# Optimization experiments

Measured on AMD Instinct MI355X. Metric: run time of the kernel, lower is better.

The kernel has to match this reference:

```python
import jax, jax.numpy as jnp
import numpy as np

B, D = 8192, 128
MARGIN = 0.1
N_CLASSES, N_GROUPS = 64, 8


def setup_inputs() -> dict:
    key = jax.random.key(0)
    k1, k2, k3 = jax.random.split(key, 3)
    embeddings = jax.random.normal(k1, (B, D), dtype=jnp.float32)
    labels = jax.random.randint(k2, (B,), 0, N_CLASSES, dtype=jnp.int64)
    groups = jax.random.randint(k3, (B,), 0, N_GROUPS, dtype=jnp.int64)
    return {"embeddings": embeddings, "labels": labels, "groups": groups}


def reference(embeddings, labels, groups):
    # cosine metric: L2-normalize rows (torch F.normalize eps=1e-12)
    norm = jnp.maximum(jnp.linalg.norm(embeddings, axis=1, keepdims=True), 1e-12)
    x = embeddings / norm
    dist = 1.0 - jnp.matmul(x, x.T)                      # [B, B]

    n = embeddings.shape[0]
    eye = jnp.eye(n, dtype=bool)
    same_label = labels[:, None] == labels[None, :]       # [B, B]
    pos_mask = same_label & ~eye
    neg_mask = ~same_label
    neg_sg_mask = neg_mask & (groups[:, None] == groups[None, :])

    BIG = jnp.float32(1e9)
    # hardest positive per row (masked max), hardest negative per row (masked min)
    dist_ap = jnp.max(jnp.where(pos_mask, dist, -BIG), axis=1)
    dist_an_sg = jnp.min(jnp.where(neg_sg_mask, dist, BIG), axis=1)
    dist_an_all = jnp.min(jnp.where(neg_mask, dist, BIG), axis=1)

    has_pos = jnp.any(pos_mask, axis=1)
    has_neg_sg = jnp.any(neg_sg_mask, axis=1)
    has_neg = jnp.any(neg_mask, axis=1)

    # fallback: same-group negatives preferred, else any negative
    dist_an = jnp.where(has_neg_sg, dist_an_sg, dist_an_all)

    loss = jax.nn.relu(dist_ap - dist_an + MARGIN)        # [B]
    # original only averages strictly-positive losses over valid anchors
    include = has_pos & has_neg & (loss > 0)
    cnt = jnp.sum(include.astype(jnp.float32))
    total = jnp.sum(jnp.where(include, loss, 0.0))
    final = jnp.where(cnt > 0, total / jnp.maximum(cnt, 1.0), 0.0)
    final = jnp.where(jnp.isnan(final), 0.0, final)
    return final
```

## Files before the change

### kernel.cpp

```cpp
#include <hip/hip_runtime.h>
#include <math.h>

#define NB 8192
#define DK 128
#define TI 128
#define NTILES (NB / TI)
#define NBLK (NTILES * (NTILES + 1) / 2)
#define JT 64
#define NT (TI / JT)
#define BSTRH 136
#define NCOMB (NB / 256)

typedef __attribute__((ext_vector_type(8))) short short8;
typedef __attribute__((ext_vector_type(16))) float float16;

__device__ inline unsigned short f2bf(float f) {
    unsigned int x = __float_as_uint(f);
    unsigned int r = (x + 0x7fffu + ((x >> 16) & 1u)) >> 16;
    return (unsigned short)r;
}

__global__ void norm_kernel(const float* __restrict__ emb, const int* __restrict__ labels,
                            const int* __restrict__ groups, unsigned short* __restrict__ xnb,
                            int* __restrict__ meta, float* __restrict__ accum,
                            int* __restrict__ ticket) {
    int row  = blockIdx.x * 4 + (threadIdx.x >> 6);
    int lane = threadIdx.x & 63;
    float2 v = ((const float2*)(emb + (size_t)row * DK))[lane];
    float ss = v.x * v.x + v.y * v.y;
#pragma unroll
    for (int off = 32; off; off >>= 1) ss += __shfl_xor(ss, off, 64);
    float inv = 1.0f / fmaxf(sqrtf(ss), 1e-12f);
    ushort2 o;
    o.x = f2bf(v.x * inv);
    o.y = f2bf(v.y * inv);
    ((ushort2*)(xnb + (size_t)row * DK))[lane] = o;
    if (lane == 0) meta[row] = (labels[row] << 8) | groups[row];
    if (blockIdx.x == 0 && threadIdx.x == 0) {
        accum[0] = 0.0f; accum[1] = 0.0f; ticket[0] = 0;
    }
}

__global__ __launch_bounds__(256, 3) void mine_tri(
    const unsigned short* __restrict__ xnb, const int* __restrict__ meta,
    float2* __restrict__ part) {
    __shared__ unsigned short Bs[JT * BSTRH];

    int bid = blockIdx.x;
    int ti = 0;
    while (bid >= NTILES - ti) { bid -= NTILES - ti; ti++; }
    const int tj = ti + bid;

    const int tid  = threadIdx.x;
    const int w    = tid >> 6;
    const int lane = tid & 63;
    const int half = lane >> 5;
    const int l31  = lane & 31;
    const int i0    = ti * TI;
    const int jbase = tj * TI;
    const int irow  = i0 + w * 32;

    short8 afrag[8];
#pragma unroll
    for (int ks = 0; ks < 8; ks++)
        afrag[ks] = *(const short8*)(xnb + (size_t)(irow + l31) * DK + ks * 16 + half * 8);

    int metaI[16];
    float apn[16], anc[16];
#pragma unroll
    for (int reg = 0; reg < 16; reg++) {
        int r = (reg & 3) + 8 * (reg >> 2) + 4 * half;
        metaI[reg] = meta[irow + r];
        apn[reg] = -1e9f; anc[reg] = -1e9f;
    }
    float apnC[4], ancC[4];
#pragma unroll
    for (int q = 0; q < 4; q++) { apnC[q] = -1e9f; ancC[q] = -1e9f; }

#pragma unroll
    for (int jt = 0; jt < NT; jt++) {
        const int j0 = jbase + jt * JT;

        if (jt) __syncthreads();
#pragma unroll
        for (int s = 0; s < 4; s++) {
            int chunk = tid + s * 256;
            int row = chunk >> 4, k4 = chunk & 15;
            *(uint4*)&Bs[row * BSTRH + k4 * 8] =
                *(const uint4*)(xnb + (size_t)(j0 + row) * DK + k4 * 8);
        }
        __syncthreads();

        int mjc[2];
        mjc[0] = meta[j0 + l31];
        mjc[1] = meta[j0 + 32 + l31];

#pragma unroll
        for (int ct = 0; ct < 2; ct++) {
            float16 c;
#pragma unroll
            for (int e = 0; e < 16; e++) c[e] = 0.0f;

            const int bro = ct * 32 + l31;
#pragma unroll
            for (int ks = 0; ks < 8; ks++) {
                short8 b = *(const short8*)&Bs[bro * BSTRH + ks * 16 + half * 8];
                c = __builtin_amdgcn_mfma_f32_32x32x16_bf16(afrag[ks], b, c, 0, 0, 0);
            }

            const int mj = mjc[ct];
            const int q  = jt * 2 + ct;
#pragma unroll
            for (int reg = 0; reg < 16; reg++) {
                float s = c[reg];
                int x = metaI[reg] ^ mj;
                bool sl = (unsigned)x < 0x100u;
                float t8 = s - 8.0f;
                float t  = sl ? t8 : s;
                float negt = -t;
                apn[reg] = fmaxf(apn[reg], negt);
                apnC[q]  = fmaxf(apnC[q],  negt);
                bool sg = (x & 0xFFu) == 0u;
                float t4 = t + 4.0f;
                float v  = sg ? t4 : t;
                anc[reg] = fmaxf(anc[reg], v);
                ancC[q]  = fmaxf(ancC[q],  v);
            }
        }
    }

#pragma unroll
    for (int reg = 0; reg < 16; reg++) {
#pragma unroll
        for (int off = 16; off; off >>= 1) {
            apn[reg] = fmaxf(apn[reg], __shfl_xor(apn[reg], off, 64));
            anc[reg] = fmaxf(anc[reg], __shfl_xor(anc[reg], off, 64));
        }
    }
    if (l31 == 0) {
#pragma unroll
        for (int reg = 0; reg < 16; reg++) {
            int r = (reg & 3) + 8 * (reg >> 2) + 4 * half;
            float2 o; o.x = apn[reg]; o.y = anc[reg];
            part[(size_t)tj * NB + (irow + r)] = o;
        }
    }

    __syncthreads();
    float* colred = (float*)&Bs[0];
#pragma unroll
    for (int q = 0; q < 4; q++) {
        apnC[q] = fmaxf(apnC[q], __shfl_xor(apnC[q], 32, 64));
        ancC[q] = fmaxf(ancC[q], __shfl_xor(ancC[q], 32, 64));
        if (half == 0) {
            colred[0 * 512 + w * 128 + q * 32 + l31] = apnC[q];
            colred[1 * 512 + w * 128 + q * 32 + l31] = ancC[q];
        }
    }
    __syncthreads();
    if (tid < 128 && ti != tj) {
        int e = tid;
        float ma = -1e9f, mn = -1e9f;
#pragma unroll
        for (int wv = 0; wv < 4; wv++) {
            ma = fmaxf(ma, colred[0 * 512 + wv * 128 + e]);
            mn = fmaxf(mn, colred[1 * 512 + wv * 128 + e]);
        }
        float2 o; o.x = ma; o.y = mn;
        part[(size_t)ti * NB + (jbase + e)] = o;
    }
}

__global__ void combine_kernel(const float2* __restrict__ part,
                               float* __restrict__ accum, int* __restrict__ ticket,
                               float* __restrict__ out) {
    int i = blockIdx.x * 256 + threadIdx.x;
    float a0 = -1e9f, a1 = -1e9f, a2 = -1e9f, a3 = -1e9f;
    float n0 = -1e9f, n1 = -1e9f, n2 = -1e9f, n3 = -1e9f;
#pragma unroll
    for (int s = 0; s < NTILES; s += 4) {
        float2 p0 = part[(size_t)(s + 0) * NB + i];
        float2 p1 = part[(size_t)(s + 1) * NB + i];
        float2 p2 = part[(size_t)(s + 2) * NB + i];
        float2 p3 = part[(size_t)(s + 3) * NB + i];
        a0 = fmaxf(a0, p0.x); n0 = fmaxf(n0, p0.y);
        a1 = fmaxf(a1, p1.x); n1 = fmaxf(n1, p1.y);
        a2 = fmaxf(a2, p2.x); n2 = fmaxf(n2, p2.y);
        a3 = fmaxf(a3, p3.x); n3 = fmaxf(n3, p3.y);
    }
    float apn = fmaxf(fmaxf(a0, a1), fmaxf(a2, a3));
    float anc = fmaxf(fmaxf(n0, n1), fmaxf(n2, n3));

    float anS = (anc > 2.0f) ? anc - 4.0f : anc;
    float loss = anS + apn - 7.9f;
    float inc = (loss > 0.0f) ? 1.0f : 0.0f;
    float val = inc * loss;

    __shared__ float ssum[4], scnt[4];
#pragma unroll
    for (int off = 32; off; off >>= 1) {
        val += __shfl_xor(val, off, 64);
        inc += __shfl_xor(inc, off, 64);
    }
    int wid = threadIdx.x >> 6, lane = threadIdx.x & 63;
    if (lane == 0) { ssum[wid] = val; scnt[wid] = inc; }
    __syncthreads();
    if (threadIdx.x == 0) {
        float s = 0.f, c = 0.f;
#pragma unroll
        for (int wv = 0; wv < 4; wv++) { s += ssum[wv]; c += scnt[wv]; }
        atomicAdd(&accum[0], s);
        atomicAdd(&accum[1], c);
        __threadfence();
        int old = atomicAdd(ticket, 1);
        if (old == gridDim.x - 1) {
            __threadfence();
            float total = __hip_atomic_load(&accum[0], __ATOMIC_RELAXED, __HIP_MEMORY_SCOPE_AGENT);
            float cnt   = __hip_atomic_load(&accum[1], __ATOMIC_RELAXED, __HIP_MEMORY_SCOPE_AGENT);
            float r = (cnt > 0.0f) ? total / fmaxf(cnt, 1.0f) : 0.0f;
            if (isnan(r)) r = 0.0f;
            out[0] = r;
        }
    }
}

extern "C" void kernel_launch(void* const* d_in, const int* in_sizes, int n_in,
                              void* d_out, int out_size, void* d_ws, size_t ws_size,
                              hipStream_t stream) {
    const float* emb  = (const float*)d_in[0];
    const int* labels = (const int*)d_in[1];
    const int* groups = (const int*)d_in[2];
    float* out = (float*)d_out;

    unsigned short* xnb = (unsigned short*)d_ws;
    int*    meta   = (int*)(xnb + (size_t)NB * DK);
    float2* part   = (float2*)(meta + NB);
    float*  accum  = (float*)(part + (size_t)NTILES * NB);
    int*    ticket = (int*)(accum + 2);

    norm_kernel<<<NB / 4, 256, 0, stream>>>(emb, labels, groups, xnb, meta, accum, ticket);
    mine_tri<<<NBLK, 256, 0, stream>>>(xnb, meta, part);
    combine_kernel<<<NCOMB, 256, 0, stream>>>(part, accum, ticket, out);
}
```

Before: 101.9 us.

## Load full B tile via direct global-to-LDS loads with XOR swizzle

Result: slower. 117.8 us (+15.5%).

```diff
diff --git a/kernel.cpp b/kernel.cpp
--- a/kernel.cpp
+++ b/kernel.cpp
@@ -6,9 +6,6 @@
 #define TI 128
 #define NTILES (NB / TI)
 #define NBLK (NTILES * (NTILES + 1) / 2)
-#define JT 64
-#define NT (TI / JT)
-#define BSTRH 136
 #define NCOMB (NB / 256)
 
 typedef __attribute__((ext_vector_type(8))) short short8;
@@ -18,6 +15,12 @@
     unsigned int x = __float_as_uint(f);
     unsigned int r = (x + 0x7fffu + ((x >> 16) & 1u)) >> 16;
     return (unsigned short)r;
+}
+
+__device__ inline void gload_lds16(const unsigned short* g, unsigned short* l) {
+    __builtin_amdgcn_global_load_lds(
+        (const __attribute__((address_space(1))) unsigned int*)g,
+        (__attribute__((address_space(3))) unsigned int*)l, 16, 0, 0);
 }
 
 __global__ void norm_kernel(const float* __restrict__ emb, const int* __restrict__ labels,
@@ -44,7 +47,7 @@
 __global__ __launch_bounds__(256, 3) void mine_tri(
     const unsigned short* __restrict__ xnb, const int* __restrict__ meta,
     float2* __restrict__ part) {
-    __shared__ unsigned short Bs[JT * BSTRH];
+    __shared__ unsigned short Bs[TI * DK];
 
     int bid = blockIdx.x;
     int ti = 0;
@@ -60,6 +63,14 @@
     const int jbase = tj * TI;
     const int irow  = i0 + w * 32;
 
+#pragma unroll
+    for (int s = 0; s < 8; s++) {
+        int slot = tid + s * 256;
+        int row  = slot >> 4;
+        int gch  = (slot & 15) ^ (row & 7);
+        gload_lds16(xnb + (size_t)(jbase + row) * DK + gch * 8, &Bs[slot * 8]);
+    }
+
     short8 afrag[8];
 #pragma unroll
     for (int ks = 0; ks < 8; ks++)
@@ -73,43 +84,34 @@
         metaI[reg] = meta[irow + r];
         apn[reg] = -1e9f; anc[reg] = -1e9f;
     }
+    int mjc[4];
+#pragma unroll
+    for (int q = 0; q < 4; q++) mjc[q] = meta[jbase + q * 32 + l31];
+
     float apnC[4], ancC[4];
 #pragma unroll
     for (int q = 0; q < 4; q++) { apnC[q] = -1e9f; ancC[q] = -1e9f; }
 
-#pragma unroll
-    for (int jt = 0; jt < NT; jt++) {
-        const int j0 = jbase + jt * JT;
-
-        if (jt) __syncthreads();
-#pragma unroll
-        for (int s = 0; s < 4; s++) {
-            int chunk = tid + s * 256;
-            int row = chunk >> 4, k4 = chunk & 15;
-            *(uint4*)&Bs[row * BSTRH + k4 * 8] =
-                *(const uint4*)(xnb + (size_t)(j0 + row) * DK + k4 * 8);
-        }
-        __syncthreads();
-
-        int mjc[2];
-        mjc[0] = meta[j0 + l31];
-        mjc[1] = meta[j0 + 32 + l31];
-
+    __syncthreads();
+
+#pragma unroll
+    for (int jt = 0; jt < 2; jt++) {
 #pragma unroll
         for (int ct = 0; ct < 2; ct++) {
+            const int q   = jt * 2 + ct;
+            const int bro = q * 32 + l31;
+
             float16 c;
 #pragma unroll
             for (int e = 0; e < 16; e++) c[e] = 0.0f;
-
-            const int bro = ct * 32 + l31;
 #pragma unroll
             for (int ks = 0; ks < 8; ks++) {
-                short8 b = *(const short8*)&Bs[bro * BSTRH + ks * 16 + half * 8];
+                int ch = ((ks * 2 + half) ^ (bro & 7)) * 8;
+                short8 b = *(const short8*)&Bs[bro * DK + ch];
                 c = __builtin_amdgcn_mfma_f32_32x32x16_bf16(afrag[ks], b, c, 0, 0, 0);
             }
 
-            const int mj = mjc[ct];
-            const int q  = jt * 2 + ct;
+            const int mj = mjc[q];
 #pragma unroll
             for (int reg = 0; reg < 16; reg++) {
                 float s = c[reg];
```
